# Optimization experiments

Measured on AMD Instinct MI355X. Metric: run time of the kernel, lower is better.

## Reference

```python
import jax, jax.numpy as jnp
import numpy as np

N = 50000      # nodes
E = 600000     # edges (avg degree 12)
D = 128        # input_dim == hidden_dim (required: same Linear reused across pool layers)
OUT = 64       # output_dim
NUM_POOL = 2   # num_pool_layers


def setup_inputs() -> dict:
    key = jax.random.key(0)
    ks = jax.random.split(key, 8)
    s = 1.0 / np.sqrt(D)  # fan-in style scaling keeps repeated scatter-adds stable
    x = jax.random.normal(ks[0], (N, D), dtype=jnp.float32)
    edge_index = jax.random.randint(ks[1], (2, E), 0, N, dtype=jnp.int64)
    W1 = jax.random.normal(ks[2], (D, D), dtype=jnp.float32) * s
    b1 = jnp.zeros((D,), dtype=jnp.float32)
    W2 = jax.random.normal(ks[3], (D, D), dtype=jnp.float32) * s
    b2 = jnp.zeros((D,), dtype=jnp.float32)
    Wout = jax.random.normal(ks[4], (D, OUT), dtype=jnp.float32) * s
    bout = jnp.zeros((OUT,), dtype=jnp.float32)
    return {"x": x, "edge_index": edge_index, "W1": W1, "b1": b1,
            "W2": W2, "b2": b2, "Wout": Wout, "bout": bout}


def _gauss_seidel_pool(x, W, b, src, dst, num_layers):
    # PyG MessagePassing(aggr='add'): out[i] = sum_{edges (j->i)} lin(x[j]).
    # Nodes with no incoming edges become zero (propagate replaces x entirely).
    for _ in range(num_layers):
        m = x @ W + b                      # [N, out] linear once per node (== lin(x_j) per edge)
        x = jax.ops.segment_sum(m[src], dst, num_segments=N)  # gather + scatter-add
    return x


def reference(x, edge_index, W1, b1, W2, b2, Wout, bout):
    src = edge_index[0]  # x_j source
    dst = edge_index[1]  # aggregation target i
    h = _gauss_seidel_pool(x, W1, b1, src, dst, NUM_POOL)
    h = jax.nn.relu(h)                     # dropout = identity (eval mode)
    h = _gauss_seidel_pool(h, W2, b2, src, dst, NUM_POOL)
    h = jax.nn.relu(h)
    return h @ Wout + bout                 # [N, OUT]
```

## Files before the change

kernel.cpp:

```cpp
#include <hip/hip_runtime.h>


static inline int ceil_div(int a, int b) { return (a + b - 1) / b; }

typedef __attribute__((ext_vector_type(8))) short bf16x8;
typedef __attribute__((ext_vector_type(4))) float f32x4;

__device__ inline unsigned short f2bf(float f) {
    unsigned u = __float_as_uint(f);
    return (unsigned short)((u + 0x7fffu + ((u >> 16) & 1u)) >> 16);
}


__device__ void wprep_dev(const float* __restrict__ W, unsigned short* __restrict__ hi,
                          int total, int C, int g0, int G) {
    for (int t = g0; t < total; t += G) {
        int j = t & 7;
        int lane = (t >> 3) & 63;
        int f = t >> 9;
        int c = f & 3, ct = f >> 2;
        int k = c * 32 + (lane >> 4) * 8 + j;
        int col = ct * 16 + (lane & 15);
        hi[t] = f2bf(W[(size_t)k * C + col]);
    }
}

__global__ __launch_bounds__(256) void prep_kernel(const float* __restrict__ W1,
                                                   const float* __restrict__ W2,
                                                   const float* __restrict__ Wout,
                                                   unsigned short* __restrict__ W1hi,
                                                   unsigned short* __restrict__ W2hi,
                                                   unsigned short* __restrict__ Wohi,
                                                   int* __restrict__ cursor,
                                                   unsigned* __restrict__ stat,
                                                   int N, int nChunks) {
    int g0 = blockIdx.x * 256 + threadIdx.x;
    int G = gridDim.x * 256;
    for (int i = g0; i < N; i += G) cursor[i] = 0;
    for (int i = g0; i < nChunks; i += G) stat[i] = 0;
    wprep_dev(W1, W1hi, 128 * 128, 128, g0, G);
    wprep_dev(W2, W2hi, 128 * 128, 128, g0, G);
    wprep_dev(Wout, Wohi, 128 * 64, 64, g0, G);
}


__global__ __launch_bounds__(256) void hist_kernel(const int* __restrict__ dst,
                                                   int* __restrict__ deg, int E) {
    int e = blockIdx.x * 256 + threadIdx.x;
    if (e < E) atomicAdd(&deg[dst[e]], 1);
}

__global__ __launch_bounds__(256) void scan_fuse_kernel(const int* __restrict__ deg,
                                                        int* __restrict__ rp,
                                                        int* __restrict__ cursor,
                                                        unsigned* __restrict__ stat,
                                                        int N) {
    __shared__ int s[256];
    int c = blockIdx.x, tid = threadIdx.x;
    int i = c * 256 + tid;
    int v = (i < N) ? deg[i] : 0;
    s[tid] = v;
    __syncthreads();
    for (int off = 1; off < 256; off <<= 1) {
        int t = (tid >= off) ? s[tid - off] : 0;
        __syncthreads();
        s[tid] += t;
        __syncthreads();
    }
    int loc = s[tid] - v;
    int tot = s[255];
    __syncthreads();
    if (tid == 0) atomicExch(&stat[c], (unsigned)tot | 0x80000000u);

    unsigned mine = 0;
    if (tid < c) {
        unsigned u;
        do { u = atomicAdd(&stat[tid], 0u); } while (!(u & 0x80000000u));
        mine = u & 0x7fffffffu;
    }
    s[tid] = (int)mine;
    __syncthreads();
    for (int off = 128; off >= 1; off >>= 1) {
        if (tid < off) s[tid] += s[tid + off];
        __syncthreads();
    }
    int prefix = s[0];
    if (i <= N) {
        int val = loc + prefix;
        rp[i] = val;
        if (i < N) cursor[i] = val;
    }
}


__global__ __launch_bounds__(256) void fill_gemm1_kernel(const int* __restrict__ src,
                                                         const int* __restrict__ dst,
                                                         int* __restrict__ cursor,
                                                         int* __restrict__ es, int E,
                                                         const float* __restrict__ X,
                                                         const uint4* __restrict__ Whi,
                                                         const float* __restrict__ Bias,
                                                         unsigned short* __restrict__ Y,
                                                         int n, int fillB) {
    int tid = threadIdx.x;
    if ((int)blockIdx.x < fillB) {
        int e = blockIdx.x * 256 + tid;
        if (e < E) {
            int p = atomicAdd(&cursor[dst[e]], 1);
            es[p] = src[e];
        }
        return;
    }

    int r0 = (blockIdx.x - fillB) * 64;
    int wave = tid >> 6, lane = tid & 63;
    int lm = lane & 15, lq = lane >> 4;

    bf16x8 afr[4][4];
#pragma unroll
    for (int rt = 0; rt < 4; ++rt) {
        int ar = r0 + rt * 16 + lm;
        if (ar > n - 1) ar = n - 1;
#pragma unroll
        for (int c = 0; c < 4; ++c) {
            int k = c * 32 + lq * 8;
            const float* ap = X + (size_t)ar * 128 + k;
            float4 f0 = ((const float4*)ap)[0];
            float4 f1 = ((const float4*)ap)[1];
            bf16x8 v;
            v[0] = (short)f2bf(f0.x); v[1] = (short)f2bf(f0.y);
            v[2] = (short)f2bf(f0.z); v[3] = (short)f2bf(f0.w);
            v[4] = (short)f2bf(f1.x); v[5] = (short)f2bf(f1.y);
            v[6] = (short)f2bf(f1.z); v[7] = (short)f2bf(f1.w);
            afr[rt][c] = v;
        }
    }

    f32x4 acc[4][2];
#pragma unroll
    for (int rt = 0; rt < 4; ++rt)
#pragma unroll
        for (int t = 0; t < 2; ++t)
            acc[rt][t] = (f32x4){0.f, 0.f, 0.f, 0.f};

#pragma unroll
    for (int c = 0; c < 4; ++c) {
#pragma unroll
        for (int t = 0; t < 2; ++t) {
            int ct = wave * 2 + t;
            uint4 uh = Whi[(ct * 4 + c) * 64 + lane];
            bf16x8 wh = *(const bf16x8*)&uh;
#pragma unroll
            for (int rt = 0; rt < 4; ++rt)
                acc[rt][t] = __builtin_amdgcn_mfma_f32_16x16x32_bf16(afr[rt][c], wh, acc[rt][t], 0, 0, 0);
        }
    }

#pragma unroll
    for (int t = 0; t < 2; ++t) {
        int col = (wave * 2 + t) * 16 + lm;
        float bias = Bias[col];
#pragma unroll
        for (int rt = 0; rt < 4; ++rt) {
#pragma unroll
            for (int r = 0; r < 4; ++r) {
                int row = r0 + rt * 16 + lq * 4 + r;
                if (row < n)
                    Y[(size_t)row * 128 + col] = f2bf(acc[rt][t][r] + bias);
            }
        }
    }
}


__device__ inline void acc_row8(float* a, uint4 v) {
    a[0] += __uint_as_float(v.x << 16);
    a[1] += __uint_as_float(v.x & 0xffff0000u);
    a[2] += __uint_as_float(v.y << 16);
    a[3] += __uint_as_float(v.y & 0xffff0000u);
    a[4] += __uint_as_float(v.z << 16);
    a[5] += __uint_as_float(v.z & 0xffff0000u);
    a[6] += __uint_as_float(v.w << 16);
    a[7] += __uint_as_float(v.w & 0xffff0000u);
}

template <int COLS, bool OUTF32>
__global__ __launch_bounds__(256) void fused_agg_gemm_kernel(const unsigned short* __restrict__ M,
                                                             const int* __restrict__ rp,
                                                             const int* __restrict__ es,
                                                             const uint4* __restrict__ Whi,
                                                             const float* __restrict__ Bias,
                                                             void* __restrict__ Yv,
                                                             int n, int do_relu) {
    constexpr int CT_W = COLS / 64;
    constexpr int SR = 136;
    __shared__ unsigned short Hl[64 * SR];

    int tid = threadIdx.x;
    int r0 = blockIdx.x * 64;

    {
        int sub = tid >> 4, ln = tid & 15;
        for (int q = 0; q < 4; ++q) {
            int nl = sub * 4 + q;
            int node = r0 + nl;
            float acc[8] = {};
            if (node < n) {
                int beg = rp[node], end = rp[node + 1];
                int e = beg;
                for (; e + 4 <= end; e += 4) {
                    int s0 = es[e], s1 = es[e + 1], s2 = es[e + 2], s3 = es[e + 3];
                    uint4 v0 = ((const uint4*)(M + (size_t)s0 * 128))[ln];
                    uint4 v1 = ((const uint4*)(M + (size_t)s1 * 128))[ln];
                    uint4 v2 = ((const uint4*)(M + (size_t)s2 * 128))[ln];
                    uint4 v3 = ((const uint4*)(M + (size_t)s3 * 128))[ln];
                    acc_row8(acc, v0);
                    acc_row8(acc, v1);
                    acc_row8(acc, v2);
                    acc_row8(acc, v3);
                }
                for (; e < end; ++e) {
                    uint4 v = ((const uint4*)(M + (size_t)es[e] * 128))[ln];
                    acc_row8(acc, v);
                }
                if (do_relu) {
#pragma unroll
                    for (int i = 0; i < 8; ++i) acc[i] = fmaxf(acc[i], 0.f);
                }
            }
            uint4 o;
            o.x = (unsigned)f2bf(acc[0]) | ((unsigned)f2bf(acc[1]) << 16);
            o.y = (unsigned)f2bf(acc[2]) | ((unsigned)f2bf(acc[3]) << 16);
            o.z = (unsigned)f2bf(acc[4]) | ((unsigned)f2bf(acc[5]) << 16);
            o.w = (unsigned)f2bf(acc[6]) | ((unsigned)f2bf(acc[7]) << 16);
            *(uint4*)(&Hl[nl * SR + ln * 8]) = o;
        }
    }
    __syncthreads();

    int wave = tid >> 6, lane = tid & 63;
    int lm = lane & 15, lq = lane >> 4;

    f32x4 acc[4][CT_W];
#pragma unroll
    for (int rt = 0; rt < 4; ++rt)
#pragma unroll
        for (int t = 0; t < CT_W; ++t)
            acc[rt][t] = (f32x4){0.f, 0.f, 0.f, 0.f};

#pragma unroll
    for (int c = 0; c < 4; ++c) {
        bf16x8 afr[4];
#pragma unroll
        for (int rt = 0; rt < 4; ++rt) {
            int nl = rt * 16 + lm;
            afr[rt] = *(const bf16x8*)(&Hl[nl * SR + c * 32 + lq * 8]);
        }
#pragma unroll
        for (int t = 0; t < CT_W; ++t) {
            int ct = wave * CT_W + t;
            uint4 uh = Whi[(ct * 4 + c) * 64 + lane];
            bf16x8 wh = *(const bf16x8*)&uh;
#pragma unroll
            for (int rt = 0; rt < 4; ++rt)
                acc[rt][t] = __builtin_amdgcn_mfma_f32_16x16x32_bf16(afr[rt], wh, acc[rt][t], 0, 0, 0);
        }
    }

#pragma unroll
    for (int t = 0; t < CT_W; ++t) {
        int col = (wave * CT_W + t) * 16 + lm;
        float bias = Bias[col];
#pragma unroll
        for (int rt = 0; rt < 4; ++rt) {
#pragma unroll
            for (int r = 0; r < 4; ++r) {
                int row = r0 + rt * 16 + lq * 4 + r;
                if (row < n) {
                    float v = acc[rt][t][r] + bias;
                    if (OUTF32)
                        ((float*)Yv)[(size_t)row * COLS + col] = v;
                    else
                        ((unsigned short*)Yv)[(size_t)row * COLS + col] = f2bf(v);
                }
            }
        }
    }
}


extern "C" void kernel_launch(void* const* d_in, const int* in_sizes, int n_in,
                              void* d_out, int out_size, void* d_ws, size_t ws_size,
                              hipStream_t stream) {
    const float* x    = (const float*)d_in[0];
    const int*   ei   = (const int*)d_in[1];
    const float* W1   = (const float*)d_in[2];
    const float* b1   = (const float*)d_in[3];
    const float* W2   = (const float*)d_in[4];
    const float* b2   = (const float*)d_in[5];
    const float* Wout = (const float*)d_in[6];
    const float* bout = (const float*)d_in[7];
    float*       out  = (float*)d_out;

    const int N = in_sizes[0] / 128;
    const int E = in_sizes[1] / 2;
    const int* src = ei;
    const int* dst = ei + E;

    char* ws = (char*)d_ws;
    auto take = [&](size_t bytes) {
        char* p = ws;
        ws += (bytes + 255) & ~(size_t)255;
        return p;
    };
    unsigned short* mA = (unsigned short*)take((size_t)N * 128 * 2);
    unsigned short* mB = (unsigned short*)take((size_t)N * 128 * 2);
    unsigned short* W1hi = (unsigned short*)take(128 * 128 * 2);
    unsigned short* W2hi = (unsigned short*)take(128 * 128 * 2);
    unsigned short* Wohi = (unsigned short*)take(128 * 64 * 2);
    int* rp      = (int*)take((size_t)(N + 1) * sizeof(int));
    int* cursor  = (int*)take((size_t)N * sizeof(int));
    int* es      = (int*)take((size_t)E * sizeof(int));
    unsigned* stat = (unsigned*)take(4096);

    const int nChunks = ceil_div(N + 1, 256);
    const int tiles = ceil_div(N, 64);
    const int fillB = ceil_div(E, 256);

    prep_kernel<<<256, 256, 0, stream>>>(W1, W2, Wout, W1hi, W2hi, Wohi,
                                         cursor, stat, N, nChunks);
    hist_kernel<<<ceil_div(E, 256), 256, 0, stream>>>(dst, cursor, E);
    scan_fuse_kernel<<<nChunks, 256, 0, stream>>>(cursor, rp, cursor, stat, N);
    fill_gemm1_kernel<<<fillB + tiles, 256, 0, stream>>>(src, dst, cursor, es, E,
                                                         x, (const uint4*)W1hi, b1,
                                                         mA, N, fillB);

    fused_agg_gemm_kernel<128, false><<<tiles, 256, 0, stream>>>(
        mA, rp, es, (const uint4*)W1hi, b1, mB, N, 0);
    fused_agg_gemm_kernel<128, false><<<tiles, 256, 0, stream>>>(
        mB, rp, es, (const uint4*)W2hi, b2, mA, N, 1);
    fused_agg_gemm_kernel<128, false><<<tiles, 256, 0, stream>>>(
        mA, rp, es, (const uint4*)W2hi, b2, mB, N, 0);
    fused_agg_gemm_kernel<64, true><<<tiles, 256, 0, stream>>>(
        mB, rp, es, (const uint4*)Wohi, bout, out, N, 1);
}
```

Baseline: 299.4 us.

## Fold two pool layers into W² with bias correction terms, fuse output GEMM

Uses linearity of the two back-to-back pool layers: A(A x W + b)W + b = A²x W² + (A·deg)(bW) + deg·b, so each pool pair becomes two plain gathers followed by one GEMM with W squared. W², the bias vectors bW and per-node degree sums are precomputed in the prep kernel. The final output projection is fused into the last pool kernel through LDS. This removes two of the four per-layer GEMMs, but adds a naive scalar W² computation in the prep kernel and extra bf16 rounding of the pre-GEMM aggregates, which may change accuracy.

```diff
diff --git a/kernel.cpp b/kernel.cpp
--- a/kernel.cpp
+++ b/kernel.cpp
@@ -12,25 +12,18 @@
 }
 
 
-__device__ void wprep_dev(const float* __restrict__ W, unsigned short* __restrict__ hi,
-                          int total, int C, int g0, int G) {
-    for (int t = g0; t < total; t += G) {
-        int j = t & 7;
-        int lane = (t >> 3) & 63;
-        int f = t >> 9;
-        int c = f & 3, ct = f >> 2;
-        int k = c * 32 + (lane >> 4) * 8 + j;
-        int col = ct * 16 + (lane & 15);
-        hi[t] = f2bf(W[(size_t)k * C + col]);
-    }
-}
-
-__global__ __launch_bounds__(256) void prep_kernel(const float* __restrict__ W1,
+__global__ __launch_bounds__(256) void prep_kernel(const float* __restrict__ x,
+                                                   const float* __restrict__ W1,
+                                                   const float* __restrict__ b1,
                                                    const float* __restrict__ W2,
+                                                   const float* __restrict__ b2,
                                                    const float* __restrict__ Wout,
-                                                   unsigned short* __restrict__ W1hi,
-                                                   unsigned short* __restrict__ W2hi,
-                                                   unsigned short* __restrict__ Wohi,
+                                                   unsigned short* __restrict__ xb,
+                                                   unsigned short* __restrict__ W1sq,
+                                                   unsigned short* __restrict__ W2sq,
+                                                   unsigned short* __restrict__ Wof,
+                                                   float* __restrict__ c1,
+                                                   float* __restrict__ c2,
                                                    int* __restrict__ cursor,
                                                    unsigned* __restrict__ stat,
                                                    int N, int nChunks) {
@@ -38,9 +31,49 @@
     int G = gridDim.x * 256;
     for (int i = g0; i < N; i += G) cursor[i] = 0;
     for (int i = g0; i < nChunks; i += G) stat[i] = 0;
-    wprep_dev(W1, W1hi, 128 * 128, 128, g0, G);
-    wprep_dev(W2, W2hi, 128 * 128, 128, g0, G);
-    wprep_dev(Wout, Wohi, 128 * 64, 64, g0, G);
+
+    int nq = N * 32;
+    for (int i = g0; i < nq; i += G) {
+        float4 v = ((const float4*)x)[i];
+        ushort4 o;
+        o.x = f2bf(v.x); o.y = f2bf(v.y); o.z = f2bf(v.z); o.w = f2bf(v.w);
+        ((ushort4*)xb)[i] = o;
+    }
+
+    for (int t = g0; t < 16384; t += G) {
+        int j = t & 7, lane = (t >> 3) & 63, f = t >> 9;
+        int c = f & 3, ct = f >> 2;
+        int k = c * 32 + (lane >> 4) * 8 + j;
+        int col = ct * 16 + (lane & 15);
+        float s = 0.f;
+        for (int u = 0; u < 128; ++u) s += W1[k * 128 + u] * W1[u * 128 + col];
+        W1sq[t] = f2bf(s);
+    }
+    for (int t = g0; t < 16384; t += G) {
+        int j = t & 7, lane = (t >> 3) & 63, f = t >> 9;
+        int c = f & 3, ct = f >> 2;
+        int k = c * 32 + (lane >> 4) * 8 + j;
+        int col = ct * 16 + (lane & 15);
+        float s = 0.f;
+        for (int u = 0; u < 128; ++u) s += W2[k * 128 + u] * W2[u * 128 + col];
+        W2sq[t] = f2bf(s);
+    }
+    for (int t = g0; t < 8192; t += G) {
+        int j = t & 7, lane = (t >> 3) & 63, f = t >> 9;
+        int c = f & 3, ct = f >> 2;
+        int k = c * 32 + (lane >> 4) * 8 + j;
+        int col = ct * 16 + (lane & 15);
+        Wof[t] = f2bf(Wout[k * 64 + col]);
+    }
+    for (int col = g0; col < 128; col += G) {
+        float s1 = 0.f, s2 = 0.f;
+        for (int k = 0; k < 128; ++k) {
+            s1 += b1[k] * W1[k * 128 + col];
+            s2 += b2[k] * W2[k * 128 + col];
+        }
+        c1[col] = s1;
+        c2[col] = s2;
+    }
 }
 
 
@@ -53,6 +86,7 @@
 __global__ __launch_bounds__(256) void scan_fuse_kernel(const int* __restrict__ deg,
                                                         int* __restrict__ rp,
                                                         int* __restrict__ cursor,
+                                                        float* __restrict__ degf,
                                                         unsigned* __restrict__ stat,
                                                         int N) {
     __shared__ int s[256];
@@ -88,87 +122,21 @@
     if (i <= N) {
         int val = loc + prefix;
         rp[i] = val;
-        if (i < N) cursor[i] = val;
-    }
-}
-
-
-__global__ __launch_bounds__(256) void fill_gemm1_kernel(const int* __restrict__ src,
-                                                         const int* __restrict__ dst,
-                                                         int* __restrict__ cursor,
-                                                         int* __restrict__ es, int E,
-                                                         const float* __restrict__ X,
-                                                         const uint4* __restrict__ Whi,
-                                                         const float* __restrict__ Bias,
-                                                         unsigned short* __restrict__ Y,
-                                                         int n, int fillB) {
-    int tid = threadIdx.x;
-    if ((int)blockIdx.x < fillB) {
-        int e = blockIdx.x * 256 + tid;
-        if (e < E) {
-            int p = atomicAdd(&cursor[dst[e]], 1);
-            es[p] = src[e];
-        }
-        return;
-    }
-
-    int r0 = (blockIdx.x - fillB) * 64;
-    int wave = tid >> 6, lane = tid & 63;
-    int lm = lane & 15, lq = lane >> 4;
-
-    bf16x8 afr[4][4];
-#pragma unroll
-    for (int rt = 0; rt < 4; ++rt) {
-        int ar = r0 + rt * 16 + lm;
-        if (ar > n - 1) ar = n - 1;
-#pragma unroll
-        for (int c = 0; c < 4; ++c) {
-            int k = c * 32 + lq * 8;
-            const float* ap = X + (size_t)ar * 128 + k;
-            float4 f0 = ((const float4*)ap)[0];
-            float4 f1 = ((const float4*)ap)[1];
-            bf16x8 v;
-            v[0] = (short)f2bf(f0.x); v[1] = (short)f2bf(f0.y);
-            v[2] = (short)f2bf(f0.z); v[3] = (short)f2bf(f0.w);
-            v[4] = (short)f2bf(f1.x); v[5] = (short)f2bf(f1.y);
-            v[6] = (short)f2bf(f1.z); v[7] = (short)f2bf(f1.w);
-            afr[rt][c] = v;
-        }
-    }
-
-    f32x4 acc[4][2];
-#pragma unroll
-    for (int rt = 0; rt < 4; ++rt)
-#pragma unroll
-        for (int t = 0; t < 2; ++t)
-            acc[rt][t] = (f32x4){0.f, 0.f, 0.f, 0.f};
-
-#pragma unroll
-    for (int c = 0; c < 4; ++c) {
-#pragma unroll
-        for (int t = 0; t < 2; ++t) {
-            int ct = wave * 2 + t;
-            uint4 uh = Whi[(ct * 4 + c) * 64 + lane];
-            bf16x8 wh = *(const bf16x8*)&uh;
-#pragma unroll
-            for (int rt = 0; rt < 4; ++rt)
-                acc[rt][t] = __builtin_amdgcn_mfma_f32_16x16x32_bf16(afr[rt][c], wh, acc[rt][t], 0, 0, 0);
-        }
-    }
-
-#pragma unroll
-    for (int t = 0; t < 2; ++t) {
-        int col = (wave * 2 + t) * 16 + lm;
-        float bias = Bias[col];
-#pragma unroll
-        for (int rt = 0; rt < 4; ++rt) {
-#pragma unroll
-            for (int r = 0; r < 4; ++r) {
-                int row = r0 + rt * 16 + lq * 4 + r;
-                if (row < n)
-                    Y[(size_t)row * 128 + col] = f2bf(acc[rt][t][r] + bias);
-            }
-        }
+        if (i < N) {
+            cursor[i] = val;
+            degf[i] = (float)v;
+        }
+    }
+}
+
+__global__ __launch_bounds__(256) void fill_kernel(const int* __restrict__ src,
+                                                   const int* __restrict__ dst,
+                                                   int* __restrict__ cursor,
+                                                   int* __restrict__ es, int E) {
+    int e = blockIdx.x * 256 + threadIdx.x;
+    if (e < E) {
+        int p = atomicAdd(&cursor[dst[e]], 1);
+        es[p] = src[e];
     }
 }
 
@@ -184,82 +152,150 @@
     a[7] += __uint_as_float(v.w & 0xffff0000u);
 }
 
-template <int COLS, bool OUTF32>
-__global__ __launch_bounds__(256) void fused_agg_gemm_kernel(const unsigned short* __restrict__ M,
-                                                             const int* __restrict__ rp,
-                                                             const int* __restrict__ es,
-                                                             const uint4* __restrict__ Whi,
-                                                             const float* __restrict__ Bias,
-                                                             void* __restrict__ Yv,
-                                                             int n, int do_relu) {
-    constexpr int CT_W = COLS / 64;
+template <bool WITH_SD>
+__global__ __launch_bounds__(256) void gather_kernel(const unsigned short* __restrict__ M,
+                                                     const int* __restrict__ rp,
+                                                     const int* __restrict__ es,
+                                                     const float* __restrict__ degf,
+                                                     unsigned short* __restrict__ Hout,
+                                                     float* __restrict__ Sd, int n) {
+    int node = blockIdx.x * 16 + (threadIdx.x >> 4);
+    int ln = threadIdx.x & 15;
+    if (node >= n) return;
+    int beg = rp[node], end = rp[node + 1];
+    float acc[8] = {};
+    float sd = 0.f;
+    int e = beg;
+    for (; e + 8 <= end; e += 8) {
+        int s0 = es[e],     s1 = es[e + 1], s2 = es[e + 2], s3 = es[e + 3];
+        int s4 = es[e + 4], s5 = es[e + 5], s6 = es[e + 6], s7 = es[e + 7];
+        uint4 v0 = ((const uint4*)(M + (size_t)s0 * 128))[ln];
+        uint4 v1 = ((const uint4*)(M + (size_t)s1 * 128))[ln];
+        uint4 v2 = ((const uint4*)(M + (size_t)s2 * 128))[ln];
+        uint4 v3 = ((const uint4*)(M + (size_t)s3 * 128))[ln];
+        uint4 v4 = ((const uint4*)(M + (size_t)s4 * 128))[ln];
+        uint4 v5 = ((const uint4*)(M + (size_t)s5 * 128))[ln];
+        uint4 v6 = ((const uint4*)(M + (size_t)s6 * 128))[ln];
+        uint4 v7 = ((const uint4*)(M + (size_t)s7 * 128))[ln];
+        if (WITH_SD)
+            sd += degf[s0] + degf[s1] + degf[s2] + degf[s3] +
+                  degf[s4] + degf[s5] + degf[s6] + degf[s7];
+        acc_row8(acc, v0); acc_row8(acc, v1); acc_row8(acc, v2); acc_row8(acc, v3);
+        acc_row8(acc, v4); acc_row8(acc, v5); acc_row8(acc, v6); acc_row8(acc, v7);
+    }
+    for (; e + 4 <= end; e += 4) {
+        int s0 = es[e], s1 = es[e + 1], s2 = es[e + 2], s3 = es[e + 3];
+        uint4 v0 = ((const uint4*)(M + (size_t)s0 * 128))[ln];
+        uint4 v1 = ((const uint4*)(M + (size_t)s1 * 128))[ln];
+        uint4 v2 = ((const uint4*)(M + (size_t)s2 * 128))[ln];
+        uint4 v3 = ((const uint4*)(M + (size_t)s3 * 128))[ln];
+        if (WITH_SD) sd += degf[s0] + degf[s1] + degf[s2] + degf[s3];
+        acc_row8(acc, v0); acc_row8(acc, v1); acc_row8(acc, v2); acc_row8(acc, v3);
+    }
+    for (; e < end; ++e) {
+        int s0 = es[e];
+        uint4 v = ((const uint4*)(M + (size_t)s0 * 128))[ln];
+        if (WITH_SD) sd += degf[s0];
+        acc_row8(acc, v);
+    }
+    uint4 o;
+    o.x = (unsigned)f2bf(acc[0]) | ((unsigned)f2bf(acc[1]) << 16);
+    o.y = (unsigned)f2bf(acc[2]) | ((unsigned)f2bf(acc[3]) << 16);
+    o.z = (unsigned)f2bf(acc[4]) | ((unsigned)f2bf(acc[5]) << 16);
+    o.w = (unsigned)f2bf(acc[6]) | ((unsigned)f2bf(acc[7]) << 16);
+    *(uint4*)(Hout + (size_t)node * 128 + ln * 8) = o;
+    if (WITH_SD && ln == 0) Sd[node] = sd;
+}
+
+
+__device__ inline void agg_tile_to_lds(const unsigned short* __restrict__ M,
+                                       const int* __restrict__ rp,
+                                       const int* __restrict__ es,
+                                       unsigned short* __restrict__ Hl,
+                                       int r0, int n, int tid) {
+    constexpr int SR = 136;
+    int sub = tid >> 4, ln = tid & 15;
+#pragma unroll 1
+    for (int q = 0; q < 4; ++q) {
+        int nl = sub * 4 + q;
+        int node = r0 + nl;
+        float acc[8] = {};
+        if (node < n) {
+            int beg = rp[node], end = rp[node + 1];
+            int e = beg;
+            for (; e + 8 <= end; e += 8) {
+                int s0 = es[e],     s1 = es[e + 1], s2 = es[e + 2], s3 = es[e + 3];
+                int s4 = es[e + 4], s5 = es[e + 5], s6 = es[e + 6], s7 = es[e + 7];
+                uint4 v0 = ((const uint4*)(M + (size_t)s0 * 128))[ln];
+                uint4 v1 = ((const uint4*)(M + (size_t)s1 * 128))[ln];
+                uint4 v2 = ((const uint4*)(M + (size_t)s2 * 128))[ln];
+                uint4 v3 = ((const uint4*)(M + (size_t)s3 * 128))[ln];
+                uint4 v4 = ((const uint4*)(M + (size_t)s4 * 128))[ln];
+                uint4 v5 = ((const uint4*)(M + (size_t)s5 * 128))[ln];
+                uint4 v6 = ((const uint4*)(M + (size_t)s6 * 128))[ln];
+                uint4 v7 = ((const uint4*)(M + (size_t)s7 * 128))[ln];
+                acc_row8(acc, v0); acc_row8(acc, v1); acc_row8(acc, v2); acc_row8(acc, v3);
+                acc_row8(acc, v4); acc_row8(acc, v5); acc_row8(acc, v6); acc_row8(acc, v7);
+            }
+            for (; e + 4 <= end; e += 4) {
+                int s0 = es[e], s1 = es[e + 1], s2 = es[e + 2], s3 = es[e + 3];
+                uint4 v0 = ((const uint4*)(M + (size_t)s0 * 128))[ln];
+                uint4 v1 = ((const uint4*)(M + (size_t)s1 * 128))[ln];
+                uint4 v2 = ((const uint4*)(M + (size_t)s2 * 128))[ln];
+                uint4 v3 = ((const uint4*)(M + (size_t)s3 * 128))[ln];
+                acc_row8(acc, v0); acc_row8(acc, v1); acc_row8(acc, v2); acc_row8(acc, v3);
+            }
+            for (; e < end; ++e) {
+                uint4 v = ((const uint4*)(M + (size_t)es[e] * 128))[ln];
+                acc_row8(acc, v);
+            }
+        }
+        uint4 o;
+        o.x = (unsigned)f2bf(acc[0]) | ((unsigned)f2bf(acc[1]) << 16);
+        o.y = (unsigned)f2bf(acc[2]) | ((unsigned)f2bf(acc[3]) << 16);
+        o.z = (unsigned)f2bf(acc[4]) | ((unsigned)f2bf(acc[5]) << 16);
+        o.w = (unsigned)f2bf(acc[6]) | ((unsigned)f2bf(acc[7]) << 16);
+        *(uint4*)(&Hl[nl * SR + ln * 8]) = o;
+    }
+}
+
+__global__ __launch_bounds__(256) void fused_pool_gemm_kernel(const unsigned short* __restrict__ M,
+                                                              const int* __restrict__ rp,
+                                                              const int* __restrict__ es,
+                                                              const uint4* __restrict__ Wf,
+                                                              const float* __restrict__ cvec,
+                                                              const float* __restrict__ bvec,
+                                                              const float* __restrict__ Sd,
+                                                              const float* __restrict__ degf,
+                                                              unsigned short* __restrict__ Y,
+                                                              int n) {
     constexpr int SR = 136;
     __shared__ unsigned short Hl[64 * SR];
-
-    int tid = threadIdx.x;
-    int r0 = blockIdx.x * 64;
-
-    {
-        int sub = tid >> 4, ln = tid & 15;
-        for (int q = 0; q < 4; ++q) {
-            int nl = sub * 4 + q;
-            int node = r0 + nl;
-            float acc[8] = {};
-            if (node < n) {
-                int beg = rp[node], end = rp[node + 1];
-                int e = beg;
-                for (; e + 4 <= end; e += 4) {
-                    int s0 = es[e], s1 = es[e + 1], s2 = es[e + 2], s3 = es[e + 3];
-                    uint4 v0 = ((const uint4*)(M + (size_t)s0 * 128))[ln];
-                    uint4 v1 = ((const uint4*)(M + (size_t)s1 * 128))[ln];
-                    uint4 v2 = ((const uint4*)(M + (size_t)s2 * 128))[ln];
-                    uint4 v3 = ((const uint4*)(M + (size_t)s3 * 128))[ln];
-                    acc_row8(acc, v0);
-                    acc_row8(acc, v1);
-                    acc_row8(acc, v2);
-                    acc_row8(acc, v3);
-                }
-                for (; e < end; ++e) {
-                    uint4 v = ((const uint4*)(M + (size_t)es[e] * 128))[ln];
-                    acc_row8(acc, v);
-                }
-                if (do_relu) {
-#pragma unroll
-                    for (int i = 0; i < 8; ++i) acc[i] = fmaxf(acc[i], 0.f);
-                }
-            }
-            uint4 o;
-            o.x = (unsigned)f2bf(acc[0]) | ((unsigned)f2bf(acc[1]) << 16);
-            o.y = (unsigned)f2bf(acc[2]) | ((unsigned)f2bf(acc[3]) << 16);
-            o.z = (unsigned)f2bf(acc[4]) | ((unsigned)f2bf(acc[5]) << 16);
-            o.w = (unsigned)f2bf(acc[6]) | ((unsigned)f2bf(acc[7]) << 16);
-            *(uint4*)(&Hl[nl * SR + ln * 8]) = o;
-        }
-    }
+    int tid = threadIdx.x, r0 = blockIdx.x * 64;
+
+    agg_tile_to_lds(M, rp, es, Hl, r0, n, tid);
     __syncthreads();
 
     int wave = tid >> 6, lane = tid & 63;
     int lm = lane & 15, lq = lane >> 4;
 
-    f32x4 acc[4][CT_W];
+    f32x4 acc[4][2];
 #pragma unroll
     for (int rt = 0; rt < 4; ++rt)
 #pragma unroll
-        for (int t = 0; t < CT_W; ++t)
+        for (int t = 0; t < 2; ++t)
             acc[rt][t] = (f32x4){0.f, 0.f, 0.f, 0.f};
 
 #pragma unroll
     for (int c = 0; c < 4; ++c) {
         bf16x8 afr[4];
 #pragma unroll
-        for (int rt = 0; rt < 4; ++rt) {
-            int nl = rt * 16 + lm;
-            afr[rt] = *(const bf16x8*)(&Hl[nl * SR + c * 32 + lq * 8]);
-        }
-#pragma unroll
-        for (int t = 0; t < CT_W; ++t) {
-            int ct = wave * CT_W + t;
-            uint4 uh = Whi[(ct * 4 + c) * 64 + lane];
+        for (int rt = 0; rt < 4; ++rt)
+            afr[rt] = *(const bf16x8*)(&Hl[(rt * 16 + lm) * SR + c * 32 + lq * 8]);
+#pragma unroll
+        for (int t = 0; t < 2; ++t) {
+            int ct = wave * 2 + t;
+            uint4 uh = Wf[(ct * 4 + c) * 64 + lane];
             bf16x8 wh = *(const bf16x8*)&uh;
 #pragma unroll
             for (int rt = 0; rt < 4; ++rt)
@@ -268,22 +304,116 @@
     }
 
 #pragma unroll
-    for (int t = 0; t < CT_W; ++t) {
-        int col = (wave * CT_W + t) * 16 + lm;
-        float bias = Bias[col];
+    for (int t = 0; t < 2; ++t) {
+        int col = (wave * 2 + t) * 16 + lm;
+        float cv = cvec[col], bv = bvec[col];
 #pragma unroll
         for (int rt = 0; rt < 4; ++rt) {
 #pragma unroll
             for (int r = 0; r < 4; ++r) {
                 int row = r0 + rt * 16 + lq * 4 + r;
                 if (row < n) {
-                    float v = acc[rt][t][r] + bias;
-                    if (OUTF32)
-                        ((float*)Yv)[(size_t)row * COLS + col] = v;
-                    else
-                        ((unsigned short*)Yv)[(size_t)row * COLS + col] = f2bf(v);
+                    float v = acc[rt][t][r] + Sd[row] * cv + degf[row] * bv;
+                    Y[(size_t)row * 128 + col] = f2bf(fmaxf(v, 0.f));
                 }
             }
+        }
+    }
+}
+
+
+__global__ __launch_bounds__(256) void fused_pool_gemm_out_kernel(const unsigned short* __restrict__ M,
+                                                                  const int* __restrict__ rp,
+                                                                  const int* __restrict__ es,
+                                                                  const uint4* __restrict__ Wf,
+                                                                  const float* __restrict__ cvec,
+                                                                  const float* __restrict__ bvec,
+                                                                  const float* __restrict__ Sd,
+                                                                  const float* __restrict__ degf,
+                                                                  const uint4* __restrict__ Wof,
+                                                                  const float* __restrict__ bout,
+                                                                  float* __restrict__ out,
+                                                                  int n) {
+    constexpr int SR = 136;
+    __shared__ unsigned short Hl[64 * SR];
+    int tid = threadIdx.x, r0 = blockIdx.x * 64;
+
+    agg_tile_to_lds(M, rp, es, Hl, r0, n, tid);
+    __syncthreads();
+
+    int wave = tid >> 6, lane = tid & 63;
+    int lm = lane & 15, lq = lane >> 4;
+
+    f32x4 acc[4][2];
+#pragma unroll
+    for (int rt = 0; rt < 4; ++rt)
+#pragma unroll
+        for (int t = 0; t < 2; ++t)
+            acc[rt][t] = (f32x4){0.f, 0.f, 0.f, 0.f};
+
+#pragma unroll
+    for (int c = 0; c < 4; ++c) {
+        bf16x8 afr[4];
+#pragma unroll
+        for (int rt = 0; rt < 4; ++rt)
+            afr[rt] = *(const bf16x8*)(&Hl[(rt * 16 + lm) * SR + c * 32 + lq * 8]);
+#pragma unroll
+        for (int t = 0; t < 2; ++t) {
+            int ct = wave * 2 + t;
+            uint4 uh = Wf[(ct * 4 + c) * 64 + lane];
+            bf16x8 wh = *(const bf16x8*)&uh;
+#pragma unroll
+            for (int rt = 0; rt < 4; ++rt)
+                acc[rt][t] = __builtin_amdgcn_mfma_f32_16x16x32_bf16(afr[rt], wh, acc[rt][t], 0, 0, 0);
+        }
+    }
+
+    __syncthreads();
+
+#pragma unroll
+    for (int t = 0; t < 2; ++t) {
+        int col = (wave * 2 + t) * 16 + lm;
+        float cv = cvec[col], bv = bvec[col];
+#pragma unroll
+        for (int rt = 0; rt < 4; ++rt) {
+#pragma unroll
+            for (int r = 0; r < 4; ++r) {
+                int rowl = rt * 16 + lq * 4 + r;
+                int row = r0 + rowl;
+                float sdv = 0.f, dv = 0.f;
+                if (row < n) { sdv = Sd[row]; dv = degf[row]; }
+                float v = acc[rt][t][r] + sdv * cv + dv * bv;
+                Hl[rowl * SR + col] = f2bf(fmaxf(v, 0.f));
+            }
+        }
+    }
+    __syncthreads();
+
+    f32x4 acc2[4];
+#pragma unroll
+    for (int rt = 0; rt < 4; ++rt) acc2[rt] = (f32x4){0.f, 0.f, 0.f, 0.f};
+
+#pragma unroll
+    for (int c = 0; c < 4; ++c) {
+        bf16x8 afr[4];
+#pragma unroll
+        for (int rt = 0; rt < 4; ++rt)
+            afr[rt] = *(const bf16x8*)(&Hl[(rt * 16 + lm) * SR + c * 32 + lq * 8]);
+        uint4 uw = Wof[(wave * 4 + c) * 64 + lane];
+        bf16x8 wf = *(const bf16x8*)&uw;
+#pragma unroll
+        for (int rt = 0; rt < 4; ++rt)
+            acc2[rt] = __builtin_amdgcn_mfma_f32_16x16x32_bf16(afr[rt], wf, acc2[rt], 0, 0, 0);
+    }
+
+    int col = wave * 16 + lm;
+    float bo = bout[col];
+#pragma unroll
+    for (int rt = 0; rt < 4; ++rt) {
+#pragma unroll
+        for (int r = 0; r < 4; ++r) {
+            int row = r0 + rt * 16 + lq * 4 + r;
+            if (row < n) out[(size_t)row * 64 + col] = acc2[rt][r] + bo;
         }
     }
 }
@@ -313,34 +443,37 @@
         ws += (bytes + 255) & ~(size_t)255;
         return p;
     };
-    unsigned short* mA = (unsigned short*)take((size_t)N * 128 * 2);
-    unsigned short* mB = (unsigned short*)take((size_t)N * 128 * 2);
-    unsigned short* W1hi = (unsigned short*)take(128 * 128 * 2);
-    unsigned short* W2hi = (unsigned short*)take(128 * 128 * 2);
-    unsigned short* Wohi = (unsigned short*)take(128 * 64 * 2);
+    unsigned short* xb = (unsigned short*)take((size_t)N * 128 * 2);
+    unsigned short* g1 = (unsigned short*)take((size_t)N * 128 * 2);
+    unsigned short* h  = (unsigned short*)take((size_t)N * 128 * 2);
+    unsigned short* g3 = (unsigned short*)take((size_t)N * 128 * 2);
+    unsigned short* W1sq = (unsigned short*)take(128 * 128 * 2);
+    unsigned short* W2sq = (unsigned short*)take(128 * 128 * 2);
+    unsigned short* Wof  = (unsigned short*)take(128 * 64 * 2);
+    float* c1   = (float*)take(128 * 4);
+    float* c2   = (float*)take(128 * 4);
+    float* Sd   = (float*)take((size_t)N * 4);
+    float* degf = (float*)take((size_t)N * 4);
     int* rp      = (int*)take((size_t)(N + 1) * sizeof(int));
     int* cursor  = (int*)take((size_t)N * sizeof(int));
     int* es      = (int*)take((size_t)E * sizeof(int));
     unsigned* stat = (unsigned*)take(4096);
 
     const int nChunks = ceil_div(N + 1, 256);
-    const int tiles = ceil_div(N, 64);
-    const int fillB = ceil_div(E, 256);
-
-    prep_kernel<<<256, 256, 0, stream>>>(W1, W2, Wout, W1hi, W2hi, Wohi,
-                                         cursor, stat, N, nChunks);
+    const int tiles   = ceil_div(N, 64);
+    const int ggrid   = ceil_div(N, 16);
+
+    prep_kernel<<<256, 256, 0, stream>>>(x, W1, b1, W2, b2, Wout, xb, W1sq, W2sq,
+                                         Wof, c1, c2, cursor, stat, N, nChunks);
     hist_kernel<<<ceil_div(E, 256), 256, 0, stream>>>(dst, cursor, E);
-    scan_fuse_kernel<<<nChunks, 256, 0, stream>>>(cursor, rp, cursor, stat, N);
-    fill_gemm1_kernel<<<fillB + tiles, 256, 0, stream>>>(src, dst, cursor, es, E,
-                                                         x, (const uint4*)W1hi, b1,
-                                                         mA, N, fillB);
-
-    fused_agg_gemm_kernel<128, false><<<tiles, 256, 0, stream>>>(
-        mA, rp, es, (const uint4*)W1hi, b1, mB, N, 0);
-    fused_agg_gemm_kernel<128, false><<<tiles, 256, 0, stream>>>(
-        mB, rp, es, (const uint4*)W2hi, b2, mA, N, 1);
-    fused_agg_gemm_kernel<128, false><<<tiles, 256, 0, stream>>>(
-        mA, rp, es, (const uint4*)W2hi, b2, mB, N, 0);
-    fused_agg_gemm_kernel<64, true><<<tiles, 256, 0, stream>>>(
-        mB, rp, es, (const uint4*)Wohi, bout, out, N, 1);
-}
+    scan_fuse_kernel<<<nChunks, 256, 0, stream>>>(cursor, rp, cursor, degf, stat, N);
+    fill_kernel<<<ceil_div(E, 256), 256, 0, stream>>>(src, dst, cursor, es, E);
+
+    gather_kernel<true><<<ggrid, 256, 0, stream>>>(xb, rp, es, degf, g1, Sd, N);
+    fused_pool_gemm_kernel<<<tiles, 256, 0, stream>>>(
+        g1, rp, es, (const uint4*)W1sq, c1, b1, Sd, degf, h, N);
+    gather_kernel<false><<<ggrid, 256, 0, stream>>>(h, rp, es, degf, g3, nullptr, N);
+    fused_pool_gemm_out_kernel<<<tiles, 256, 0, stream>>>(
+        g3, rp, es, (const uint4*)W2sq, c2, b2, Sd, degf,
+        (const uint4*)Wof, bout, out, N);
+}
```

Result: slower. 323.8 us (+8.1%).

## Use 16-bit edge indices, 32-row aggregation tiles, deeper gather unroll

Applied to the files above, without the earlier changes.

Stores the CSR source indices as unsigned short instead of int, which halves index traffic but only works while the node count stays below 65536. The fused aggregate+GEMM kernel now handles 32 rows per block instead of 64, doubling the grid and halving shared memory per block. The neighbour gather loop gains an 8-wide unrolled stage so more row loads are in flight at once. The combined fill/GEMM1 kernel is split into two separate launches, which gives up their overlap in exchange for simpler kernels.

```diff
diff --git a/kernel.cpp b/kernel.cpp
--- a/kernel.cpp
+++ b/kernel.cpp
@@ -92,29 +92,26 @@
     }
 }
 
-
-__global__ __launch_bounds__(256) void fill_gemm1_kernel(const int* __restrict__ src,
-                                                         const int* __restrict__ dst,
-                                                         int* __restrict__ cursor,
-                                                         int* __restrict__ es, int E,
-                                                         const float* __restrict__ X,
-                                                         const uint4* __restrict__ Whi,
-                                                         const float* __restrict__ Bias,
-                                                         unsigned short* __restrict__ Y,
-                                                         int n, int fillB) {
+__global__ __launch_bounds__(256) void fill_kernel(const int* __restrict__ src,
+                                                   const int* __restrict__ dst,
+                                                   int* __restrict__ cursor,
+                                                   unsigned short* __restrict__ es, int E) {
+    int e = blockIdx.x * 256 + threadIdx.x;
+    if (e < E) {
+        int p = atomicAdd(&cursor[dst[e]], 1);
+        es[p] = (unsigned short)src[e];
+    }
+}
+
+
+__global__ __launch_bounds__(256) void gemm1_kernel(const float* __restrict__ X,
+                                                    const uint4* __restrict__ Whi,
+                                                    const float* __restrict__ Bias,
+                                                    unsigned short* __restrict__ Y, int n) {
     int tid = threadIdx.x;
-    if ((int)blockIdx.x < fillB) {
-        int e = blockIdx.x * 256 + tid;
-        if (e < E) {
-            int p = atomicAdd(&cursor[dst[e]], 1);
-            es[p] = src[e];
-        }
-        return;
-    }
-
-    int r0 = (blockIdx.x - fillB) * 64;
     int wave = tid >> 6, lane = tid & 63;
     int lm = lane & 15, lq = lane >> 4;
+    int r0 = blockIdx.x * 64;
 
     bf16x8 afr[4][4];
 #pragma unroll
@@ -187,37 +184,52 @@
 template <int COLS, bool OUTF32>
 __global__ __launch_bounds__(256) void fused_agg_gemm_kernel(const unsigned short* __restrict__ M,
                                                              const int* __restrict__ rp,
-                                                             const int* __restrict__ es,
+                                                             const unsigned short* __restrict__ es,
                                                              const uint4* __restrict__ Whi,
                                                              const float* __restrict__ Bias,
                                                              void* __restrict__ Yv,
                                                              int n, int do_relu) {
     constexpr int CT_W = COLS / 64;
     constexpr int SR = 136;
-    __shared__ unsigned short Hl[64 * SR];
+    __shared__ unsigned short Hl[32 * SR];
 
     int tid = threadIdx.x;
-    int r0 = blockIdx.x * 64;
+    int r0 = blockIdx.x * 32;
 
     {
         int sub = tid >> 4, ln = tid & 15;
-        for (int q = 0; q < 4; ++q) {
-            int nl = sub * 4 + q;
+#pragma unroll 1
+        for (int q = 0; q < 2; ++q) {
+            int nl = sub * 2 + q;
             int node = r0 + nl;
             float acc[8] = {};
             if (node < n) {
                 int beg = rp[node], end = rp[node + 1];
                 int e = beg;
+                for (; e + 8 <= end; e += 8) {
+                    int s0 = es[e],     s1 = es[e + 1], s2 = es[e + 2], s3 = es[e + 3];
+                    int s4 = es[e + 4], s5 = es[e + 5], s6 = es[e + 6], s7 = es[e + 7];
+                    uint4 v0 = ((const uint4*)(M + (size_t)s0 * 128))[ln];
+                    uint4 v1 = ((const uint4*)(M + (size_t)s1 * 128))[ln];
+                    uint4 v2 = ((const uint4*)(M + (size_t)s2 * 128))[ln];
+                    uint4 v3 = ((const uint4*)(M + (size_t)s3 * 128))[ln];
+                    uint4 v4 = ((const uint4*)(M + (size_t)s4 * 128))[ln];
+                    uint4 v5 = ((const uint4*)(M + (size_t)s5 * 128))[ln];
+                    uint4 v6 = ((const uint4*)(M + (size_t)s6 * 128))[ln];
+                    uint4 v7 = ((const uint4*)(M + (size_t)s7 * 128))[ln];
+                    acc_row8(acc, v0); acc_row8(acc, v1);
+                    acc_row8(acc, v2); acc_row8(acc, v3);
+                    acc_row8(acc, v4); acc_row8(acc, v5);
+                    acc_row8(acc, v6); acc_row8(acc, v7);
+                }
                 for (; e + 4 <= end; e += 4) {
                     int s0 = es[e], s1 = es[e + 1], s2 = es[e + 2], s3 = es[e + 3];
                     uint4 v0 = ((const uint4*)(M + (size_t)s0 * 128))[ln];
                     uint4 v1 = ((const uint4*)(M + (size_t)s1 * 128))[ln];
                     uint4 v2 = ((const uint4*)(M + (size_t)s2 * 128))[ln];
                     uint4 v3 = ((const uint4*)(M + (size_t)s3 * 128))[ln];
-                    acc_row8(acc, v0);
-                    acc_row8(acc, v1);
-                    acc_row8(acc, v2);
-                    acc_row8(acc, v3);
+                    acc_row8(acc, v0); acc_row8(acc, v1);
+                    acc_row8(acc, v2); acc_row8(acc, v3);
                 }
                 for (; e < end; ++e) {
                     uint4 v = ((const uint4*)(M + (size_t)es[e] * 128))[ln];
@@ -241,28 +253,26 @@
     int wave = tid >> 6, lane = tid & 63;
     int lm = lane & 15, lq = lane >> 4;
 
-    f32x4 acc[4][CT_W];
-#pragma unroll
-    for (int rt = 0; rt < 4; ++rt)
+    f32x4 acc[2][CT_W];
+#pragma unroll
+    for (int rt = 0; rt < 2; ++rt)
 #pragma unroll
         for (int t = 0; t < CT_W; ++t)
             acc[rt][t] = (f32x4){0.f, 0.f, 0.f, 0.f};
 
 #pragma unroll
     for (int c = 0; c < 4; ++c) {
-        bf16x8 afr[4];
-#pragma unroll
-        for (int rt = 0; rt < 4; ++rt) {
-            int nl = rt * 16 + lm;
-            afr[rt] = *(const bf16x8*)(&Hl[nl * SR + c * 32 + lq * 8]);
-        }
+        bf16x8 afr[2];
+#pragma unroll
+        for (int rt = 0; rt < 2; ++rt)
+            afr[rt] = *(const bf16x8*)(&Hl[(rt * 16 + lm) * SR + c * 32 + lq * 8]);
 #pragma unroll
         for (int t = 0; t < CT_W; ++t) {
             int ct = wave * CT_W + t;
             uint4 uh = Whi[(ct * 4 + c) * 64 + lane];
             bf16x8 wh = *(const bf16x8*)&uh;
 #pragma unroll
-            for (int rt = 0; rt < 4; ++rt)
+            for (int rt = 0; rt < 2; ++rt)
                 acc[rt][t] = __builtin_amdgcn_mfma_f32_16x16x32_bf16(afr[rt], wh, acc[rt][t], 0, 0, 0);
         }
     }
@@ -272,7 +282,7 @@
         int col = (wave * CT_W + t) * 16 + lm;
         float bias = Bias[col];
 #pragma unroll
-        for (int rt = 0; rt < 4; ++rt) {
+        for (int rt = 0; rt < 2; ++rt) {
 #pragma unroll
             for (int r = 0; r < 4; ++r) {
                 int row = r0 + rt * 16 + lq * 4 + r;
@@ -320,27 +330,26 @@
     unsigned short* Wohi = (unsigned short*)take(128 * 64 * 2);
     int* rp      = (int*)take((size_t)(N + 1) * sizeof(int));
     int* cursor  = (int*)take((size_t)N * sizeof(int));
-    int* es      = (int*)take((size_t)E * sizeof(int));
+    unsigned short* es = (unsigned short*)take((size_t)E * sizeof(unsigned short));
     unsigned* stat = (unsigned*)take(4096);
 
     const int nChunks = ceil_div(N + 1, 256);
-    const int tiles = ceil_div(N, 64);
-    const int fillB = ceil_div(E, 256);
+    const int tiles64 = ceil_div(N, 64);
+    const int tiles32 = ceil_div(N, 32);
 
     prep_kernel<<<256, 256, 0, stream>>>(W1, W2, Wout, W1hi, W2hi, Wohi,
                                          cursor, stat, N, nChunks);
     hist_kernel<<<ceil_div(E, 256), 256, 0, stream>>>(dst, cursor, E);
     scan_fuse_kernel<<<nChunks, 256, 0, stream>>>(cursor, rp, cursor, stat, N);
-    fill_gemm1_kernel<<<fillB + tiles, 256, 0, stream>>>(src, dst, cursor, es, E,
-                                                         x, (const uint4*)W1hi, b1,
-                                                         mA, N, fillB);
-
-    fused_agg_gemm_kernel<128, false><<<tiles, 256, 0, stream>>>(
+    fill_kernel<<<ceil_div(E, 256), 256, 0, stream>>>(src, dst, cursor, es, E);
+    gemm1_kernel<<<tiles64, 256, 0, stream>>>(x, (const uint4*)W1hi, b1, mA, N);
+
+    fused_agg_gemm_kernel<128, false><<<tiles32, 256, 0, stream>>>(
         mA, rp, es, (const uint4*)W1hi, b1, mB, N, 0);
-    fused_agg_gemm_kernel<128, false><<<tiles, 256, 0, stream>>>(
+    fused_agg_gemm_kernel<128, false><<<tiles32, 256, 0, stream>>>(
         mB, rp, es, (const uint4*)W2hi, b2, mA, N, 1);
-    fused_agg_gemm_kernel<128, false><<<tiles, 256, 0, stream>>>(
+    fused_agg_gemm_kernel<128, false><<<tiles32, 256, 0, stream>>>(
         mA, rp, es, (const uint4*)W2hi, b2, mB, N, 0);
-    fused_agg_gemm_kernel<64, true><<<tiles, 256, 0, stream>>>(
+    fused_agg_gemm_kernel<64, true><<<tiles32, 256, 0, stream>>>(
         mB, rp, es, (const uint4*)Wohi, bout, out, N, 1);
 }
```

New measurement: 299.7 us. About the same (+0.1%).
